# Optimization experiments

Measured on AMD Instinct MI355X. Metric: run time of the kernel, lower is better.

Reference implementation:

```python
import jax, jax.numpy as jnp
import numpy as np

THRESHOLD = 0.5
NEG_POS = 3
ALPHA = 1.0


def cxcy_to_xy(c):
    return jnp.concatenate([c[..., :2] - c[..., 2:] / 2, c[..., :2] + c[..., 2:] / 2], axis=-1)


def xy_to_cxcy(x):
    return jnp.concatenate([(x[..., :2] + x[..., 2:]) / 2, x[..., 2:] - x[..., :2]], axis=-1)


def encode_gcxgcy(cxcy, priors_cxcy):
    # SSD offset encoding with variances (10, 10, 5, 5)
    return jnp.concatenate([
        (cxcy[..., :2] - priors_cxcy[..., :2]) / (priors_cxcy[..., 2:] / 10.0),
        jnp.log(cxcy[..., 2:] / priors_cxcy[..., 2:]) * 5.0,
    ], axis=-1)


def compute_iou(a, b):
    # a: [n,4] xyxy, b: [m,4] xyxy -> [n,m]
    lt = jnp.maximum(a[:, None, :2], b[None, :, :2])
    rb = jnp.minimum(a[:, None, 2:], b[None, :, 2:])
    wh = jnp.clip(rb - lt, 0.0)
    inter = wh[..., 0] * wh[..., 1]
    area_a = (a[:, 2] - a[:, 0]) * (a[:, 3] - a[:, 1])
    area_b = (b[:, 2] - b[:, 0]) * (b[:, 3] - b[:, 1])
    return inter / (area_a[:, None] + area_b[None, :] - inter)


def _match_one(boxes, labels, db_xy, db_cxcy):
    # boxes: [n_obj,4] xyxy, labels: [n_obj], priors: [P,4]
    n_obj = boxes.shape[0]
    overlaps = compute_iou(boxes, db_xy)                 # [n_obj, P]
    ov_per_box = jnp.max(overlaps, axis=0)               # [P]
    obj_per_box = jnp.argmax(overlaps, axis=0)           # [P]
    box_per_obj = jnp.argmax(overlaps, axis=1)           # [n_obj]
    # force each gt to own its best prior
    obj_per_box = obj_per_box.at[box_per_obj].set(jnp.arange(n_obj))
    ov_per_box = ov_per_box.at[box_per_obj].set(1.0)
    lbl = labels[obj_per_box]                            # [P]
    lbl = jnp.where(ov_per_box < THRESHOLD, 0, lbl)      # background below threshold
    true_locs = encode_gcxgcy(xy_to_cxcy(boxes[obj_per_box]), db_cxcy)  # [P,4]
    return true_locs, lbl


def smooth_l1(x):
    ax = jnp.abs(x)
    return jnp.where(ax < 1.0, 0.5 * x * x, ax - 0.5)


def reference(loc_pred, cls_pred, gt_boxes, gt_labels, default_boxes):
    # loc_pred: [B,P,4], cls_pred: [B,P,C], gt_boxes: [B,n_obj,4],
    # gt_labels: [B,n_obj] int, default_boxes: [P,4] cxcywh
    db_xy = cxcy_to_xy(default_boxes)
    true_locs, true_labels = jax.vmap(_match_one, in_axes=(0, 0, None, None))(
        gt_boxes, gt_labels, db_xy, default_boxes)      # [B,P,4], [B,P]

    positive = true_labels > 0                           # [B,P]
    n_pos = jnp.sum(positive, axis=1)                    # [B]
    n_pos_total = jnp.sum(n_pos).astype(loc_pred.dtype)

    # localization loss: SmoothL1 mean over positive box elements
    loc_elem = smooth_l1(loc_pred - true_locs)           # [B,P,4]
    loc_loss = jnp.sum(loc_elem * positive[..., None]) / (n_pos_total * 4.0)

    # confidence loss: cross entropy with 3:1 hard negative mining
    logp = jax.nn.log_softmax(cls_pred, axis=-1)         # [B,P,C]
    ce = -jnp.take_along_axis(logp, true_labels[..., None], axis=-1)[..., 0]  # [B,P]
    conf_pos = jnp.sum(ce * positive)
    ce_neg = jnp.where(positive, 0.0, ce)
    # rank negatives by loss (descending) per image; take top neg_pos * n_pos
    ranks = jnp.argsort(jnp.argsort(-ce_neg, axis=1), axis=1)  # [B,P]
    hard_neg = ranks < (NEG_POS * n_pos)[:, None]
    conf_hard = jnp.sum(ce_neg * hard_neg)
    conf_loss = (conf_pos + conf_hard) / n_pos_total

    return conf_loss + ALPHA * loc_loss


def setup_inputs() -> dict:
    key = jax.random.key(0)
    ks = jax.random.split(key, 8)
    B, P, C, n_obj = 64, 8732, 81, 32

    # priors in cxcywh, valid in [0,1]
    db_cxy = jax.random.uniform(ks[0], (P, 2), minval=0.05, maxval=0.95)
    db_wh = jax.random.uniform(ks[1], (P, 2), minval=0.05, maxval=0.3)
    default_boxes = jnp.concatenate([db_cxy, db_wh], axis=-1).astype(jnp.float32)

    # gt boxes: valid xyxy built from centers and sizes
    g_cxy = jax.random.uniform(ks[2], (B, n_obj, 2), minval=0.2, maxval=0.8)
    g_wh = jax.random.uniform(ks[3], (B, n_obj, 2), minval=0.1, maxval=0.4)
    gt_boxes = jnp.concatenate([g_cxy - g_wh / 2, g_cxy + g_wh / 2], axis=-1).astype(jnp.float32)
    gt_labels = jax.random.randint(ks[4], (B, n_obj), 1, C)

    loc_pred = jax.random.normal(ks[5], (B, P, 4), dtype=jnp.float32) * 0.1
    cls_pred = jax.random.normal(ks[6], (B, P, C), dtype=jnp.float32)

    return {"loc_pred": loc_pred, "cls_pred": cls_pred, "gt_boxes": gt_boxes,
            "gt_labels": gt_labels, "default_boxes": default_boxes}
```

## Files before the change

### kernel.cpp

```cpp
#include <hip/hip_runtime.h>
#include <hip/hip_bf16.h>
#include <math.h>

#define BB 64
#define PP 8732
#define CC 81
#define NOBJ 32
#define CHUNKS ((PP + 255) / 256)
#define NPRI (BB * PP)
#define WTILE 16
#define WTW (WTILE * CC)
#define NWT (NPRI / WTILE)
#define LSE_BLOCKS 1792
#define BP_BLOCKS (BB * (NOBJ / 4))
#define PRE_BLOCKS (BP_BLOCKS + LSE_BLOCKS)

typedef float f4 __attribute__((ext_vector_type(4)));

__device__ __forceinline__ float sl1(float x) {
    float ax = fabsf(x);
    return (ax < 1.0f) ? 0.5f * x * x : ax - 0.5f;
}

__global__ __launch_bounds__(256) void k_pre(
    const float* __restrict__ gt_boxes,
    const float* __restrict__ dbox,
    const float* __restrict__ cls_pred,
    int*   __restrict__ bp,
    float* __restrict__ lse,
    float* __restrict__ acc,
    int*   __restrict__ npt,
    int*   __restrict__ done,
    int*   __restrict__ n_pos)
{
    __shared__ float s_x[4][WTW];
    const int tid  = threadIdx.x;
    const int wave = tid >> 6, lane = tid & 63;

    if (blockIdx.x == 0) {
        if (tid < BB) n_pos[tid] = 0;
        else if (tid < BB + 3) acc[tid - BB] = 0.0f;
        else if (tid == BB + 3) *npt = 0;
        else if (tid == BB + 4) *done = 0;
    }

    if (blockIdx.x < BP_BLOCKS) {
        const int b = blockIdx.x >> 3;
        const int o = ((blockIdx.x & 7) << 2) + wave;

        const float* g = gt_boxes + (b * NOBJ + o) * 4;
        float gx0 = g[0], gy0 = g[1], gx1 = g[2], gy1 = g[3];
        float garea = (gx1 - gx0) * (gy1 - gy0);

        float best = -1.0f; int bpp = 0x7fffffff;
        for (int p = lane; p < PP; p += 64) {
            float4 db = reinterpret_cast<const float4*>(dbox)[p];
            float px0 = db.x - db.z * 0.5f, py0 = db.y - db.w * 0.5f;
            float px1 = db.x + db.z * 0.5f, py1 = db.y + db.w * 0.5f;
            float parea = db.z * db.w;
            float lx = fmaxf(px0, gx0), ly = fmaxf(py0, gy0);
            float rx = fminf(px1, gx1), ry = fminf(py1, gy1);
            float w = fmaxf(rx - lx, 0.0f), h = fmaxf(ry - ly, 0.0f);
            float inter = w * h;
            float iou = inter / (garea + parea - inter);
            if (iou > best) { best = iou; bpp = p; }
        }
#pragma unroll
        for (int m = 32; m > 0; m >>= 1) {
            float ov = __shfl_xor(best, m);
            int   op = __shfl_xor(bpp, m);
            if (ov > best || (ov == best && op < bpp)) { best = ov; bpp = op; }
        }
        if (lane == 0) bp[b * NOBJ + o] = bpp;
        return;
    }

    const int rloc = lane >> 2, q = lane & 3;
    const int NW   = LSE_BLOCKS * 4;
    float* sx = s_x[wave];
    f4* dst = reinterpret_cast<f4*>(sx);

    const float L2E = 1.4426950408889634f;
    const float LN2 = 0.6931471805599453f;

    int wt = (blockIdx.x - BP_BLOCKS) * 4 + wave;
    f4 r0, r1, r2, r3, r4, r5;
    if (wt < NWT) {
        const f4* src = reinterpret_cast<const f4*>(cls_pred + (size_t)wt * WTW);
        r0 = __builtin_nontemporal_load(src + lane);
        r1 = __builtin_nontemporal_load(src + 64 + lane);
        r2 = __builtin_nontemporal_load(src + 128 + lane);
        r3 = __builtin_nontemporal_load(src + 192 + lane);
        r4 = __builtin_nontemporal_load(src + 256 + lane);
        if (lane < 4) r5 = __builtin_nontemporal_load(src + 320 + lane);
    }

    while (wt < NWT) {
        dst[lane] = r0; dst[64 + lane] = r1; dst[128 + lane] = r2;
        dst[192 + lane] = r3; dst[256 + lane] = r4;
        if (lane < 4) dst[320 + lane] = r5;
        const int pidx = wt * WTILE + rloc;

        wt += NW;
        if (wt < NWT) {
            const f4* src = reinterpret_cast<const f4*>(cls_pred + (size_t)wt * WTW);
            r0 = __builtin_nontemporal_load(src + lane);
            r1 = __builtin_nontemporal_load(src + 64 + lane);
            r2 = __builtin_nontemporal_load(src + 128 + lane);
            r3 = __builtin_nontemporal_load(src + 192 + lane);
            r4 = __builtin_nontemporal_load(src + 256 + lane);
            if (lane < 4) r5 = __builtin_nontemporal_load(src + 320 + lane);
        }

        const float* x = sx + rloc * CC;
        const int base = q * 20;
        float s0 = 0.0f, s1 = 0.0f;
#pragma unroll
        for (int j = 0; j < 20; j += 2) {
            s0 += exp2f(x[base + j]     * L2E);
            s1 += exp2f(x[base + j + 1] * L2E);
        }
        float s = s0 + s1;
        if (q == 3) s += exp2f(x[80] * L2E);
        s += __shfl_xor(s, 1);
        s += __shfl_xor(s, 2);

        if (q == 0) lse[pidx] = log2f(s) * LN2;
    }
}

__global__ __launch_bounds__(256) void k_assign(
    const float* __restrict__ loc_pred,
    const float* __restrict__ gt_boxes,
    const int*   __restrict__ gt_labels,
    const float* __restrict__ dbox,
    const int*   __restrict__ bp,
    int*   __restrict__ true_label,
    int*   __restrict__ n_pos,
    float* __restrict__ acc,
    int*   __restrict__ n_pos_total)
{
    __shared__ float s_gx0[NOBJ], s_gy0[NOBJ], s_gx1[NOBJ], s_gy1[NOBJ], s_garea[NOBJ];
    __shared__ float s_gcx[NOBJ], s_gcy[NOBJ], s_gw[NOBJ], s_gh[NOBJ];
    __shared__ int   s_glbl[NOBJ], s_bp[NOBJ];
    __shared__ float red_f[256];
    __shared__ int   red_i[256];

    const int b     = blockIdx.x / CHUNKS;
    const int chunk = blockIdx.x % CHUNKS;
    const int tid   = threadIdx.x;
    const int p     = chunk * 256 + tid;

    if (tid < NOBJ) {
        float x0 = gt_boxes[(b * NOBJ + tid) * 4 + 0];
        float y0 = gt_boxes[(b * NOBJ + tid) * 4 + 1];
        float x1 = gt_boxes[(b * NOBJ + tid) * 4 + 2];
        float y1 = gt_boxes[(b * NOBJ + tid) * 4 + 3];
        s_gx0[tid] = x0; s_gy0[tid] = y0; s_gx1[tid] = x1; s_gy1[tid] = y1;
        s_garea[tid] = (x1 - x0) * (y1 - y0);
        s_gcx[tid] = (x0 + x1) * 0.5f;
        s_gcy[tid] = (y0 + y1) * 0.5f;
        s_gw[tid]  = x1 - x0;
        s_gh[tid]  = y1 - y0;
        s_glbl[tid] = gt_labels[b * NOBJ + tid];
        s_bp[tid]   = bp[b * NOBJ + tid];
    }
    __syncthreads();

    float loc_local = 0.0f;
    int   np_local  = 0;

    if (p < PP) {
        float4 db = reinterpret_cast<const float4*>(dbox)[p];
        float px0 = db.x - db.z * 0.5f, py0 = db.y - db.w * 0.5f;
        float px1 = db.x + db.z * 0.5f, py1 = db.y + db.w * 0.5f;
        float parea = db.z * db.w;

        float best = -1.0f; int bo = 0;
#pragma unroll
        for (int o = 0; o < NOBJ; ++o) {
            float lx = fmaxf(px0, s_gx0[o]), ly = fmaxf(py0, s_gy0[o]);
            float rx = fminf(px1, s_gx1[o]), ry = fminf(py1, s_gy1[o]);
            float w = fmaxf(rx - lx, 0.0f), h = fmaxf(ry - ly, 0.0f);
            float inter = w * h;
            float iou = inter / (s_garea[o] + parea - inter);
            if (iou > best) { best = iou; bo = o; }
        }
        int forced = -1;
#pragma unroll
        for (int o = 0; o < NOBJ; ++o)
            if (s_bp[o] == p) forced = o;

        int o_use, lbl;
        if (forced >= 0) { o_use = forced; lbl = s_glbl[forced]; }
        else             { o_use = bo; lbl = (best < 0.5f) ? 0 : s_glbl[bo]; }

        true_label[b * PP + p] = lbl;
        if (lbl > 0) {
            np_local = 1;
            float g0 = (s_gcx[o_use] - db.x) / (db.z / 10.0f);
            float g1 = (s_gcy[o_use] - db.y) / (db.w / 10.0f);
            float g2 = logf(s_gw[o_use] / db.z) * 5.0f;
            float g3 = logf(s_gh[o_use] / db.w) * 5.0f;
            float4 lp = reinterpret_cast<const float4*>(loc_pred)[b * PP + p];
            loc_local = sl1(lp.x - g0) + sl1(lp.y - g1) + sl1(lp.z - g2) + sl1(lp.w - g3);
        }
    }

    red_f[tid] = loc_local;
    red_i[tid] = np_local;
    __syncthreads();
#pragma unroll
    for (int st = 128; st > 0; st >>= 1) {
        if (tid < st) { red_f[tid] += red_f[tid + st]; red_i[tid] += red_i[tid + st]; }
        __syncthreads();
    }
    if (tid == 0) {
        atomicAdd(&acc[0], red_f[0]);
        atomicAdd(&n_pos[b], red_i[0]);
        atomicAdd(n_pos_total, red_i[0]);
    }
}

__global__ __launch_bounds__(1024) void k_select(
    const float* __restrict__ cls_pred,
    const float* __restrict__ lse,
    const int*   __restrict__ true_label,
    const int*   __restrict__ n_pos,
    float* __restrict__ acc,
    const int*  __restrict__ n_pos_total,
    int*   __restrict__ done,
    float* __restrict__ out)
{
    __shared__ unsigned int sv[PP];
    __shared__ unsigned int hist[257];
    __shared__ unsigned int wtot[4];
    __shared__ unsigned int s_prefix, s_krem;
    __shared__ float red_f[1024];
    __shared__ int   red_i[1024];

    const int b = blockIdx.x, tid = threadIdx.x, lane = tid & 63;

    float pos_local = 0.0f;
    for (int i = tid; i < PP; i += 1024) {
        const int idx = b * PP + i;
        float l = lse[idx];
        int lbl = true_label[idx];
        float xl = cls_pred[(size_t)idx * CC + lbl];
        float ce = fmaxf(l - xl, 0.0f);
        if (lbl > 0) { pos_local += ce; sv[i] = 0u; }
        else sv[i] = __float_as_uint(ce);
    }
    red_f[tid] = pos_local;
    __syncthreads();
#pragma unroll
    for (int st = 512; st > 0; st >>= 1) {
        if (tid < st) red_f[tid] += red_f[tid + st];
        __syncthreads();
    }
    if (tid == 0 && red_f[0] != 0.0f) atomicAdd(&acc[1], red_f[0]);
    __syncthreads();

    int K = n_pos[b] * 3;
    if (K > PP) K = PP;

    if (K > 0) {
        unsigned int prefix = 0, krem = (unsigned int)K;
        for (int shift = 24; shift >= 0; shift -= 8) {
            if (tid < 256) hist[tid] = 0;
            if (tid == 0) hist[256] = 0;
            __syncthreads();
            unsigned int mask_hi = (shift == 24) ? 0u : (0xFFFFFFFFu << (shift + 8));
            for (int i = tid; i < PP; i += 1024) {
                unsigned int v = sv[i];
                if ((v & mask_hi) == prefix) atomicAdd(&hist[(v >> shift) & 0xFFu], 1u);
            }
            __syncthreads();
            unsigned int s = 0;
            if (tid < 256) {
                s = hist[tid];
#pragma unroll
                for (int off = 1; off < 64; off <<= 1) {
                    unsigned int a = __shfl_down(s, off);
                    if (lane + off < 64) s += a;
                }
                if (lane == 0) wtot[tid >> 6] = s;
            }
            __syncthreads();
            if (tid < 256) {
                for (int w2 = (tid >> 6) + 1; w2 < 4; ++w2) s += wtot[w2];
                hist[tid] = s;
            }
            __syncthreads();
            if (tid < 256) {
                unsigned int suf  = hist[tid];
                unsigned int suf1 = hist[tid + 1];
                if (suf >= krem && suf1 < krem) {
                    s_prefix = prefix | ((unsigned int)tid << shift);
                    s_krem   = krem - suf1;
                }
            }
            __syncthreads();
            prefix = s_prefix; krem = s_krem;
        }
        float cutoff = __uint_as_float(prefix);

        float sum_gt = 0.0f; int cnt_gt = 0;
        for (int i = tid; i < PP; i += 1024) {
            float v = __uint_as_float(sv[i]);
            if (v > cutoff) { sum_gt += v; cnt_gt++; }
        }
        red_f[tid] = sum_gt; red_i[tid] = cnt_gt;
        __syncthreads();
#pragma unroll
        for (int st = 512; st > 0; st >>= 1) {
            if (tid < st) { red_f[tid] += red_f[tid + st]; red_i[tid] += red_i[tid + st]; }
            __syncthreads();
        }
        if (tid == 0)
            atomicAdd(&acc[2], red_f[0] + (float)(K - red_i[0]) * cutoff);
    }

    if (tid == 0) {
        __threadfence();
        int old = atomicAdd(done, 1);
        if (old == BB - 1) {
            float a0 = atomicAdd(&acc[0], 0.0f);
            float a1 = atomicAdd(&acc[1], 0.0f);
            float a2 = atomicAdd(&acc[2], 0.0f);
            float npt = (float)atomicAdd((int*)n_pos_total, 0);
            out[0] = (a1 + a2) / npt + a0 / (npt * 4.0f);
        }
    }
}

extern "C" void kernel_launch(void* const* d_in, const int* in_sizes, int n_in,
                              void* d_out, int out_size, void* d_ws, size_t ws_size,
                              hipStream_t stream) {
    const float* loc_pred  = (const float*)d_in[0];
    const float* cls_pred  = (const float*)d_in[1];
    const float* gt_boxes  = (const float*)d_in[2];
    const int*   gt_labels = (const int*)d_in[3];
    const float* dbox      = (const float*)d_in[4];
    float* out = (float*)d_out;

    float* acc        = (float*)d_ws;
    int*   npt        = (int*)d_ws + 3;
    int*   done       = (int*)d_ws + 4;
    int*   n_pos      = (int*)d_ws + 8;
    int*   bp         = (int*)d_ws + 8 + BB;
    int*   true_label = (int*)d_ws + 8 + BB + BB * NOBJ;
    float* lse        = (float*)((int*)d_ws + 8 + BB + BB * NOBJ + (size_t)NPRI);

    k_pre<<<PRE_BLOCKS, 256, 0, stream>>>(gt_boxes, dbox, cls_pred,
                                          bp, lse, acc, npt, done, n_pos);
    k_assign<<<BB * CHUNKS, 256, 0, stream>>>(loc_pred, gt_boxes, gt_labels, dbox, bp,
                                              true_label, n_pos, acc, npt);
    k_select<<<BB, 1024, 0, stream>>>(cls_pred, lse, true_label, n_pos,
                                      acc, npt, done, out);
}
```

Before: 177.2 us.

## Move per-prior cross-entropy gather from k_select into k_assign

The gather of the true-class logit, the cross-entropy computation and the positive-loss accumulation move from the 64-block k_select into the widely parallel k_assign kernel. k_assign writes negative CE values (zero for positives) to a buffer, and k_select only loads them into shared memory when K>0. This takes the scattered cls_pred gathers out of a low-occupancy kernel and drops the true_label round trip. In exchange k_assign does more memory work, and the atomics are now skipped when a partial sum is zero.

```diff
diff --git a/kernel.cpp b/kernel.cpp
--- a/kernel.cpp
+++ b/kernel.cpp
@@ -135,7 +135,9 @@
     const int*   __restrict__ gt_labels,
     const float* __restrict__ dbox,
     const int*   __restrict__ bp,
-    int*   __restrict__ true_label,
+    const float* __restrict__ cls_pred,
+    const float* __restrict__ lse,
+    float* __restrict__ ce_neg,
     int*   __restrict__ n_pos,
     float* __restrict__ acc,
     int*   __restrict__ n_pos_total)
@@ -143,7 +145,7 @@
     __shared__ float s_gx0[NOBJ], s_gy0[NOBJ], s_gx1[NOBJ], s_gy1[NOBJ], s_garea[NOBJ];
     __shared__ float s_gcx[NOBJ], s_gcy[NOBJ], s_gw[NOBJ], s_gh[NOBJ];
     __shared__ int   s_glbl[NOBJ], s_bp[NOBJ];
-    __shared__ float red_f[256];
+    __shared__ float red_f[256], red_g[256];
     __shared__ int   red_i[256];
 
     const int b     = blockIdx.x / CHUNKS;
@@ -167,10 +169,11 @@
     }
     __syncthreads();
 
-    float loc_local = 0.0f;
+    float loc_local = 0.0f, pos_local = 0.0f;
     int   np_local  = 0;
 
     if (p < PP) {
+        const int idx = b * PP + p;
         float4 db = reinterpret_cast<const float4*>(dbox)[p];
         float px0 = db.x - db.z * 0.5f, py0 = db.y - db.w * 0.5f;
         float px1 = db.x + db.z * 0.5f, py1 = db.y + db.w * 0.5f;
@@ -195,37 +198,49 @@
         if (forced >= 0) { o_use = forced; lbl = s_glbl[forced]; }
         else             { o_use = bo; lbl = (best < 0.5f) ? 0 : s_glbl[bo]; }
 
-        true_label[b * PP + p] = lbl;
+        float xl = cls_pred[(size_t)idx * CC + lbl];
+        float ce = fmaxf(lse[idx] - xl, 0.0f);
+
         if (lbl > 0) {
             np_local = 1;
+            pos_local = ce;
+            ce_neg[idx] = 0.0f;
             float g0 = (s_gcx[o_use] - db.x) / (db.z / 10.0f);
             float g1 = (s_gcy[o_use] - db.y) / (db.w / 10.0f);
             float g2 = logf(s_gw[o_use] / db.z) * 5.0f;
             float g3 = logf(s_gh[o_use] / db.w) * 5.0f;
-            float4 lp = reinterpret_cast<const float4*>(loc_pred)[b * PP + p];
+            float4 lp = reinterpret_cast<const float4*>(loc_pred)[idx];
             loc_local = sl1(lp.x - g0) + sl1(lp.y - g1) + sl1(lp.z - g2) + sl1(lp.w - g3);
+        } else {
+            ce_neg[idx] = ce;
         }
     }
 
     red_f[tid] = loc_local;
+    red_g[tid] = pos_local;
     red_i[tid] = np_local;
     __syncthreads();
 #pragma unroll
     for (int st = 128; st > 0; st >>= 1) {
-        if (tid < st) { red_f[tid] += red_f[tid + st]; red_i[tid] += red_i[tid + st]; }
+        if (tid < st) {
+            red_f[tid] += red_f[tid + st];
+            red_g[tid] += red_g[tid + st];
+            red_i[tid] += red_i[tid + st];
+        }
         __syncthreads();
     }
     if (tid == 0) {
-        atomicAdd(&acc[0], red_f[0]);
-        atomicAdd(&n_pos[b], red_i[0]);
-        atomicAdd(n_pos_total, red_i[0]);
+        if (red_f[0] != 0.0f) atomicAdd(&acc[0], red_f[0]);
+        if (red_g[0] != 0.0f) atomicAdd(&acc[1], red_g[0]);
+        if (red_i[0]) {
+            atomicAdd(&n_pos[b], red_i[0]);
+            atomicAdd(n_pos_total, red_i[0]);
+        }
     }
 }
 
 __global__ __launch_bounds__(1024) void k_select(
-    const float* __restrict__ cls_pred,
-    const float* __restrict__ lse,
-    const int*   __restrict__ true_label,
+    const float* __restrict__ ce_neg,
     const int*   __restrict__ n_pos,
     float* __restrict__ acc,
     const int*  __restrict__ n_pos_total,
@@ -241,30 +256,14 @@
 
     const int b = blockIdx.x, tid = threadIdx.x, lane = tid & 63;
 
-    float pos_local = 0.0f;
-    for (int i = tid; i < PP; i += 1024) {
-        const int idx = b * PP + i;
-        float l = lse[idx];
-        int lbl = true_label[idx];
-        float xl = cls_pred[(size_t)idx * CC + lbl];
-        float ce = fmaxf(l - xl, 0.0f);
-        if (lbl > 0) { pos_local += ce; sv[i] = 0u; }
-        else sv[i] = __float_as_uint(ce);
-    }
-    red_f[tid] = pos_local;
-    __syncthreads();
-#pragma unroll
-    for (int st = 512; st > 0; st >>= 1) {
-        if (tid < st) red_f[tid] += red_f[tid + st];
-        __syncthreads();
-    }
-    if (tid == 0 && red_f[0] != 0.0f) atomicAdd(&acc[1], red_f[0]);
-    __syncthreads();
-
     int K = n_pos[b] * 3;
     if (K > PP) K = PP;
 
     if (K > 0) {
+        for (int i = tid; i < PP; i += 1024)
+            sv[i] = __float_as_uint(ce_neg[b * PP + i]);
+        __syncthreads();
+
         unsigned int prefix = 0, krem = (unsigned int)K;
         for (int shift = 24; shift >= 0; shift -= 8) {
             if (tid < 256) hist[tid] = 0;
@@ -344,18 +343,17 @@
     const float* dbox      = (const float*)d_in[4];
     float* out = (float*)d_out;
 
-    float* acc        = (float*)d_ws;
-    int*   npt        = (int*)d_ws + 3;
-    int*   done       = (int*)d_ws + 4;
-    int*   n_pos      = (int*)d_ws + 8;
-    int*   bp         = (int*)d_ws + 8 + BB;
-    int*   true_label = (int*)d_ws + 8 + BB + BB * NOBJ;
-    float* lse        = (float*)((int*)d_ws + 8 + BB + BB * NOBJ + (size_t)NPRI);
+    float* acc    = (float*)d_ws;
+    int*   npt    = (int*)d_ws + 3;
+    int*   done   = (int*)d_ws + 4;
+    int*   n_pos  = (int*)d_ws + 8;
+    int*   bp     = (int*)d_ws + 8 + BB;
+    float* lse    = (float*)((int*)d_ws + 8 + BB + BB * NOBJ);
+    float* ce_neg = lse + (size_t)NPRI;
 
     k_pre<<<PRE_BLOCKS, 256, 0, stream>>>(gt_boxes, dbox, cls_pred,
                                           bp, lse, acc, npt, done, n_pos);
     k_assign<<<BB * CHUNKS, 256, 0, stream>>>(loc_pred, gt_boxes, gt_labels, dbox, bp,
-                                              true_label, n_pos, acc, npt);
-    k_select<<<BB, 1024, 0, stream>>>(cls_pred, lse, true_label, n_pos,
-                                      acc, npt, done, out);
-}
+                                              cls_pred, lse, ce_neg, n_pos, acc, npt);
+    k_select<<<BB, 1024, 0, stream>>>(ce_neg, n_pos, acc, npt, done, out);
+}
```

After: 181.7 us. 2.6% more time.
